# Kernel tuning notes

Measured on AMD Instinct MI355X. Metric: run time of the kernel, lower is better.

The kernel has to match this reference:

```python
import jax, jax.numpy as jnp
import numpy as np

N, E = 100000, 640000
IN, H, C, L = 128, 128, 64, 5
BN_EPS = 1e-5


def setup_inputs() -> dict:
    key = jax.random.key(0)
    ks = jax.random.split(key, 12)
    x = jax.random.normal(ks[0], (N, IN), jnp.float32)
    edge_index = jax.random.randint(ks[1], (2, E), 0, N, dtype=jnp.int64)
    # GCNConv weights: layer0 in->hidden, layers 1..4 hidden->hidden
    W_in = jax.random.normal(ks[2], (IN, H), jnp.float32) / np.sqrt(IN).astype(np.float32)
    b_in = jnp.zeros((H,), jnp.float32)
    Ws = jax.random.normal(ks[3], (L - 1, H, H), jnp.float32) / np.sqrt(H).astype(np.float32)
    bs = jnp.zeros((L - 1, H), jnp.float32)
    # BatchNorm1d (eval mode) params per layer
    gammas = jnp.ones((L, H), jnp.float32)
    betas = jnp.zeros((L, H), jnp.float32)
    run_mean = 0.1 * jax.random.normal(ks[4], (L, H), jnp.float32)
    run_var = jax.random.uniform(ks[5], (L, H), jnp.float32) + 0.5
    # final node-level classifier
    W_out = jax.random.normal(ks[6], (H, C), jnp.float32) / np.sqrt(H).astype(np.float32)
    b_out = jnp.zeros((C,), jnp.float32)
    return {"x": x, "edge_index": edge_index, "W_in": W_in, "b_in": b_in,
            "Ws": Ws, "bs": bs, "gammas": gammas, "betas": betas,
            "run_mean": run_mean, "run_var": run_var, "W_out": W_out, "b_out": b_out}


def reference(x, edge_index, W_in, b_in, Ws, bs, gammas, betas, run_mean, run_var, W_out, b_out):
    src, dst = edge_index[0], edge_index[1]
    n = x.shape[0]
    # GCN symmetric norm with self-loops: deg counts incoming edges + 1
    deg = jax.ops.segment_sum(jnp.ones(src.shape, x.dtype), dst, num_segments=n) + 1.0
    dis = jax.lax.rsqrt(deg)                      # deg^{-1/2}, [N]
    coef = dis[src] * dis[dst]                    # per-edge norm, [E]
    self_coef = (dis * dis)[:, None]              # self-loop norm deg^{-1}, [N,1]

    h = x
    for l in range(L):
        W = W_in if l == 0 else Ws[l - 1]
        b = b_in if l == 0 else bs[l - 1]
        t = h @ W                                 # [N,H]
        agg = jax.ops.segment_sum(t[src] * coef[:, None], dst, num_segments=n)
        agg = agg + t * self_coef + b             # neighbor agg + self loop + bias
        # BatchNorm1d in eval mode (running stats)
        y = (agg - run_mean[l]) * jax.lax.rsqrt(run_var[l] + BN_EPS) * gammas[l] + betas[l]
        h = jax.nn.relu(y)                        # dropout is identity in eval
    return h @ W_out + b_out                      # [N, num_classes]
```

## Files before the change

### kernel.cpp

```cpp
#include <hip/hip_runtime.h>
#include <cstdint>

#define BN_EPS 1e-5f

typedef __bf16 bf16x8 __attribute__((ext_vector_type(8)));
typedef __bf16 bf16x4 __attribute__((ext_vector_type(4)));
typedef __bf16 bf16x2 __attribute__((ext_vector_type(2)));
typedef float f32x4 __attribute__((ext_vector_type(4)));


__global__ __launch_bounds__(256) void k_count(const int* __restrict__ dstv,
                                               int* __restrict__ counts,
                                               int* __restrict__ rank, int E) {
  int e = blockIdx.x * 256 + threadIdx.x;
  if (e < E) rank[e] = atomicAdd(counts + dstv[e], 1);
}

__global__ __launch_bounds__(256) void k_dis(const int* __restrict__ counts,
                                             float* __restrict__ dis, int N) {
  int i = blockIdx.x * 256 + threadIdx.x;
  if (i < N) dis[i] = rsqrtf((float)counts[i] + 1.0f);
}

__global__ __launch_bounds__(256) void k_scan1(const int* __restrict__ counts,
                                               int* __restrict__ rowstart,
                                               int* __restrict__ bsum, int N) {
  __shared__ int wsum[4];
  const int tid = threadIdx.x, lane = tid & 63, wv = tid >> 6;
  const int base = blockIdx.x * 1024 + tid * 4;
  int c[4];
#pragma unroll
  for (int j = 0; j < 4; ++j) {
    int idx = base + j;
    c[j] = (idx < N) ? counts[idx] : 0;
  }
  int s = c[0] + c[1] + c[2] + c[3];
  int x = s;
  for (int d = 1; d < 64; d <<= 1) {
    int y = __shfl_up(x, d);
    if (lane >= d) x += y;
  }
  if (lane == 63) wsum[wv] = x;
  __syncthreads();
  int woff = 0;
  for (int w = 0; w < wv; ++w) woff += wsum[w];
  int r = woff + x - s;
#pragma unroll
  for (int j = 0; j < 4; ++j) {
    int idx = base + j;
    if (idx < N) rowstart[idx] = r;
    r += c[j];
  }
  if (tid == 255) bsum[blockIdx.x] = woff + x;
}

__global__ __launch_bounds__(256) void k_scan2(const int* __restrict__ bsum,
                                               int* __restrict__ boff, int nb) {
  __shared__ int sm[256];
  const int tid = threadIdx.x;
  int v = (tid < nb) ? bsum[tid] : 0;
  sm[tid] = v;
  __syncthreads();
  for (int d = 1; d < 256; d <<= 1) {
    int y = (tid >= d) ? sm[tid - d] : 0;
    __syncthreads();
    sm[tid] += y;
    __syncthreads();
  }
  if (tid < nb) boff[tid] = sm[tid] - v;
}

__global__ __launch_bounds__(256) void k_fix(int* __restrict__ rowstart,
                                             const int* __restrict__ boff, int N) {
  int i = blockIdx.x * 256 + threadIdx.x;
  if (i < N) rowstart[i] += boff[i >> 10];
}

__global__ __launch_bounds__(256) void k_scatter(const int* __restrict__ src,
                                                 const int* __restrict__ dstv,
                                                 const int* __restrict__ rowstart,
                                                 const int* __restrict__ rank,
                                                 int* __restrict__ esrc, int E) {
  int e = blockIdx.x * 256 + threadIdx.x;
  if (e < E) esrc[rowstart[dstv[e]] + rank[e]] = src[e];
}

__global__ __launch_bounds__(256) void k_bnparam(const float* __restrict__ gamma,
                                                 const float* __restrict__ beta,
                                                 const float* __restrict__ mean,
                                                 const float* __restrict__ var,
                                                 float* __restrict__ scale,
                                                 float* __restrict__ shift, int n) {
  int i = blockIdx.x * 256 + threadIdx.x;
  if (i < n) {
    float s = gamma[i] * rsqrtf(var[i] + BN_EPS);
    scale[i] = s;
    shift[i] = beta[i] - mean[i] * s;
  }
}

__global__ __launch_bounds__(64) void k_zrow(__bf16* __restrict__ t, int N) {
  bf16x2 z;
  z[0] = (__bf16)0.f;
  z[1] = (__bf16)0.f;
  *reinterpret_cast<bf16x2*>(t + (size_t)N * 128 + threadIdx.x * 2) = z;
}

__global__ __launch_bounds__(256) void k_wprep(const float* __restrict__ W_in,
                                               const float* __restrict__ Ws,
                                               const float* __restrict__ W_out,
                                               __bf16* __restrict__ wfrag) {
  const int idx = blockIdx.x * 256 + threadIdx.x;
  if (idx >= 11264) return;
  int l, r, CT;
  if (idx < 10240) { l = idx >> 11; r = idx & 2047; CT = 8; }
  else             { l = 5; r = idx - 10240; CT = 4; }
  const int lane = r & 63;
  const int rr = r >> 6;
  const int ct = rr % CT;
  const int kc_i = rr / CT;
  const int lr = lane & 15, kg = lane >> 4;
  const int col = ct * 16 + lr;
  const int k0 = kc_i * 32 + kg * 8;
  const float* Wsrc;
  int ncols;
  if (l == 0)      { Wsrc = W_in; ncols = 128; }
  else if (l <= 4) { Wsrc = Ws + (size_t)(l - 1) * 16384; ncols = 128; }
  else             { Wsrc = W_out; ncols = 64; }
  bf16x8 hi, lo;
#pragma unroll
  for (int j = 0; j < 8; ++j) {
    float v = Wsrc[(size_t)(k0 + j) * ncols + col];
    __bf16 h = (__bf16)v;
    hi[j] = h;
    lo[j] = (__bf16)(v - (float)h);
  }
  const size_t lbase = (l < 5) ? (size_t)l * 65536 : (size_t)327680;
  char* outp = (char*)wfrag + lbase;
  *(bf16x8*)(outp + ((size_t)(kc_i * 2 + 0) * CT + ct) * 1024 + lane * 16) = hi;
  *(bf16x8*)(outp + ((size_t)(kc_i * 2 + 1) * CT + ct) * 1024 + lane * 16) = lo;
}

__global__ __launch_bounds__(256, 4) void k_mgemm0(
    const float* __restrict__ in, const __bf16* __restrict__ wfrag,
    const float* __restrict__ dis, __bf16* __restrict__ outh, int N) {
  constexpr int CT = 8;
  __shared__ __align__(16) char Abase[32768];

  const int tid = threadIdx.x;
  const int lane = tid & 63;
  const int wv = tid >> 6;
  const int lr = lane & 15;
  const int kg = lane >> 4;
  const int rowBase = blockIdx.x * 128;

  {
    const int kq = tid & 31;
#pragma unroll
    for (int i = 0; i < 16; ++i) {
      const int row = (tid >> 5) + i * 8;
      const int grow = rowBase + row;
      float4 v = make_float4(0.f, 0.f, 0.f, 0.f);
      if (grow < N) v = *(const float4*)(in + (size_t)grow * 128 + kq * 4);
      bf16x4 h;
      h[0] = (__bf16)v.x; h[1] = (__bf16)v.y; h[2] = (__bf16)v.z; h[3] = (__bf16)v.w;
      int byte = row * 256 + kq * 8;
      byte ^= (row & 7) << 4;
      *(bf16x4*)(Abase + byte) = h;
    }
  }
  __syncthreads();

  f32x4 acc[2][CT] = {};
#pragma unroll
  for (int kc_i = 0; kc_i < 4; ++kc_i) {
    bf16x8 afr[2];
#pragma unroll
    for (int rt = 0; rt < 2; ++rt) {
      const int row = wv * 32 + rt * 16 + lr;
      int byte = row * 256 + kc_i * 64 + kg * 16;
      byte ^= (row & 7) << 4;
      afr[rt] = *(const bf16x8*)(Abase + byte);
    }
    const char* wk = (const char*)wfrag + (size_t)kc_i * (2 * CT * 1024) +
                     (size_t)lane * 16;
#pragma unroll
    for (int ct = 0; ct < CT; ++ct) {
      bf16x8 bhi = *(const bf16x8*)(wk + ct * 1024);
      bf16x8 blo = *(const bf16x8*)(wk + (CT + ct) * 1024);
#pragma unroll
      for (int rt = 0; rt < 2; ++rt) {
        acc[rt][ct] = __builtin_amdgcn_mfma_f32_16x16x32_bf16(afr[rt], bhi,
                                                              acc[rt][ct], 0, 0, 0);
        acc[rt][ct] = __builtin_amdgcn_mfma_f32_16x16x32_bf16(afr[rt], blo,
                                                              acc[rt][ct], 0, 0, 0);
      }
    }
  }

#pragma unroll
  for (int rt = 0; rt < 2; ++rt) {
#pragma unroll
    for (int j = 0; j < 4; ++j) {
      const int row = rowBase + wv * 32 + rt * 16 + kg * 4 + j;
      if (row < N) {
        const float dr = dis[row];
#pragma unroll
        for (int ct = 0; ct < CT; ++ct)
          outh[(size_t)row * 128 + ct * 16 + lr] = (__bf16)(acc[rt][ct][j] * dr);
      }
    }
  }
}

template <int CT, bool FINAL>
__global__ __launch_bounds__(256, 6) void k_layer(
    const __bf16* __restrict__ tin, const __bf16* __restrict__ wfrag,
    const int* __restrict__ rowstart, const int* __restrict__ counts,
    const int* __restrict__ esrc, const float* __restrict__ dis,
    const float* __restrict__ bias, const float* __restrict__ scale,
    const float* __restrict__ shift, const float* __restrict__ out_bias,
    float* __restrict__ outf, __bf16* __restrict__ outh, int N) {
  __shared__ __align__(16) char Abase[16384];

  const int tid = threadIdx.x;
  const int lane = tid & 63;
  const int wv = tid >> 6;
  const int lr = lane & 15;
  const int kg = lane >> 4;
  const int rowBase = blockIdx.x * 64;

  {
    const int nb0 = rowBase + wv * 16;
    int mb = 0, mc = 0, mdbits = 0;
    if (lane < 16) {
      const int nd = nb0 + lane;
      if (nd < N) {
        mb = rowstart[nd];
        mc = counts[nd];
        mdbits = __float_as_int(dis[nd]);
      }
    }
    const int f0 = lane * 2;
    const float bx = bias[f0], by = bias[f0 + 1];
    const float scx = scale[f0], scy = scale[f0 + 1];
    const float shx = shift[f0], shy = shift[f0 + 1];

    int ci = __builtin_amdgcn_readlane(mc, 0);
    int rec = (lane < ci) ? esrc[__builtin_amdgcn_readlane(mb, 0) + lane] : N;

    for (int i = 0; i < 16; ++i) {
      const int node = nb0 + i;
      const float dn = __int_as_float(__builtin_amdgcn_readlane(mdbits, i));
      const int srow = (node < N) ? node : N;
      const bf16x2 sv =
          *reinterpret_cast<const bf16x2*>(tin + (size_t)srow * 128 + f0);
      int rec_n = N, cn = 0;
      if (i < 15) {
        const int bn_ = __builtin_amdgcn_readlane(mb, i + 1);
        cn = __builtin_amdgcn_readlane(mc, i + 1);
        if (lane < cn) rec_n = esrc[bn_ + lane];
      }
      float ax = (float)sv[0];
      float ay = (float)sv[1];
      const int m = ci < 64 ? ci : 64;
      const int rounds = (m + 7) >> 3;
      for (int r = 0; r < rounds; ++r) {
        const int rb = r * 8;
#pragma unroll
        for (int u = 0; u < 8; ++u) {
          const int s = __builtin_amdgcn_readlane(rec, rb + u);
          const bf16x2 v =
              *reinterpret_cast<const bf16x2*>(tin + (size_t)s * 128 + f0);
          ax += (float)v[0];
          ay += (float)v[1];
        }
      }
      if (__builtin_expect(ci > 64, 0)) {
        const int bi = __builtin_amdgcn_readlane(mb, i);
        for (int e = 64; e < ci; ++e) {
          const int s0 = esrc[bi + e];
          const bf16x2 v0 =
              *reinterpret_cast<const bf16x2*>(tin + (size_t)s0 * 128 + f0);
          ax += (float)v0[0];
          ay += (float)v0[1];
        }
      }
      ax = fmaf(ax, dn, bx);
      ay = fmaf(ay, dn, by);
      ax = fmaxf(fmaf(ax, scx, shx), 0.f);
      ay = fmaxf(fmaf(ay, scy, shy), 0.f);
      bf16x2 o;
      o[0] = (__bf16)ax;
      o[1] = (__bf16)ay;
      const int row = wv * 16 + i;
      int byte = row * 256 + lane * 4;
      byte ^= (row & 7) << 4;
      *(bf16x2*)(Abase + byte) = o;
      rec = rec_n;
      ci = cn;
    }
  }
  __threadfence_block();

  f32x4 acc[CT] = {};
#pragma unroll
  for (int kc_i = 0; kc_i < 4; ++kc_i) {
    const int row = wv * 16 + lr;
    int byte = row * 256 + kc_i * 64 + kg * 16;
    byte ^= (row & 7) << 4;
    const bf16x8 afr = *(const bf16x8*)(Abase + byte);
    const char* wk = (const char*)wfrag + (size_t)kc_i * (2 * CT * 1024) +
                     (size_t)lane * 16;
#pragma unroll
    for (int ct = 0; ct < CT; ++ct) {
      bf16x8 bhi = *(const bf16x8*)(wk + ct * 1024);
      bf16x8 blo = *(const bf16x8*)(wk + (CT + ct) * 1024);
      acc[ct] = __builtin_amdgcn_mfma_f32_16x16x32_bf16(afr, bhi, acc[ct], 0, 0, 0);
      acc[ct] = __builtin_amdgcn_mfma_f32_16x16x32_bf16(afr, blo, acc[ct], 0, 0, 0);
    }
  }

  float ob[CT];
  if constexpr (FINAL) {
#pragma unroll
    for (int ct = 0; ct < CT; ++ct) ob[ct] = out_bias[ct * 16 + lr];
  }
#pragma unroll
  for (int j = 0; j < 4; ++j) {
    const int row = rowBase + wv * 16 + kg * 4 + j;
    if (row < N) {
      if constexpr (FINAL) {
#pragma unroll
        for (int ct = 0; ct < CT; ++ct)
          outf[(size_t)row * (CT * 16) + ct * 16 + lr] = acc[ct][j] + ob[ct];
      } else {
        const float dr = dis[row];
#pragma unroll
        for (int ct = 0; ct < CT; ++ct)
          outh[(size_t)row * 128 + ct * 16 + lr] = (__bf16)(acc[ct][j] * dr);
      }
    }
  }
}

extern "C" void kernel_launch(void* const* d_in, const int* in_sizes, int n_in,
                              void* d_out, int out_size, void* d_ws, size_t ws_size,
                              hipStream_t stream) {
  const float* x      = (const float*)d_in[0];
  const int*   ei     = (const int*)d_in[1];
  const float* W_in   = (const float*)d_in[2];
  const float* b_in   = (const float*)d_in[3];
  const float* Ws     = (const float*)d_in[4];
  const float* bs     = (const float*)d_in[5];
  const float* gammas = (const float*)d_in[6];
  const float* betas  = (const float*)d_in[7];
  const float* mean   = (const float*)d_in[8];
  const float* var    = (const float*)d_in[9];
  const float* W_out  = (const float*)d_in[10];
  const float* b_out  = (const float*)d_in[11];
  float* out = (float*)d_out;

  const int N = in_sizes[0] / 128;
  const int E = in_sizes[1] / 2;
  const int* src = ei;
  const int* dst = ei + E;

  char* ws = (char*)d_ws;
  size_t off = 0;
  auto alloc = [&](size_t bytes) {
    void* p = ws + off;
    off = (off + bytes + 255) & ~255ULL;
    return p;
  };
  int*    counts   = (int*)alloc((size_t)N * 4);
  int*    rowstart = (int*)alloc((size_t)N * 4);
  int*    bsum     = (int*)alloc(256 * 4);
  int*    boff     = (int*)alloc(256 * 4);
  float*  dis      = (float*)alloc((size_t)N * 4);
  float*  scale    = (float*)alloc(5 * 128 * 4);
  float*  shift    = (float*)alloc(5 * 128 * 4);
  __bf16* wfrag    = (__bf16*)alloc(360448);
  int*    rank     = (int*)alloc((size_t)E * 4);
  int*    esrc     = (int*)alloc((size_t)E * 4);
  __bf16* tA       = (__bf16*)alloc(((size_t)N + 1) * 128 * 2);
  __bf16* tB       = (__bf16*)alloc(((size_t)N + 1) * 128 * 2);
  (void)ws_size;

  const int nb = (N + 1023) / 1024;

  hipMemsetAsync(counts, 0, (size_t)N * 4, stream);
  k_count<<<(E + 255) / 256, 256, 0, stream>>>(dst, counts, rank, E);
  k_dis<<<(N + 255) / 256, 256, 0, stream>>>(counts, dis, N);
  k_scan1<<<nb, 256, 0, stream>>>(counts, rowstart, bsum, N);
  k_scan2<<<1, 256, 0, stream>>>(bsum, boff, nb);
  k_fix<<<(N + 255) / 256, 256, 0, stream>>>(rowstart, boff, N);
  k_scatter<<<(E + 255) / 256, 256, 0, stream>>>(src, dst, rowstart, rank, esrc, E);
  k_bnparam<<<(5 * 128 + 255) / 256, 256, 0, stream>>>(gammas, betas, mean, var,
                                                       scale, shift, 5 * 128);
  k_wprep<<<44, 256, 0, stream>>>(W_in, Ws, W_out, wfrag);
  k_zrow<<<1, 64, 0, stream>>>(tA, N);
  k_zrow<<<1, 64, 0, stream>>>(tB, N);

  const int gblocks = (N + 127) / 128;
  const int lblocks = (N + 63) / 64;

  k_mgemm0<<<gblocks, 256, 0, stream>>>(x, wfrag, dis, tA, N);

  const float* biases[5] = {b_in, bs, bs + 128, bs + 256, bs + 384};
  __bf16* tin = tA;
  __bf16* tout = tB;
  for (int l = 1; l <= 4; ++l) {
    k_layer<8, false><<<lblocks, 256, 0, stream>>>(
        tin, wfrag + (size_t)l * 32768, rowstart, counts, esrc, dis,
        biases[l - 1], scale + (l - 1) * 128, shift + (l - 1) * 128, nullptr,
        nullptr, tout, N);
    __bf16* tmp = tin;
    tin = tout;
    tout = tmp;
  }
  k_layer<4, true><<<lblocks, 256, 0, stream>>>(
      tin, wfrag + 163840, rowstart, counts, esrc, dis, biases[4],
      scale + 4 * 128, shift + 4 * 128, b_out, out, nullptr, N);
}
```

Before: 293.4 us.

## Merge setup kernels and gather two nodes' neighbors concurrently in layer kernel

Folds degree-normalization into the scan kernel and combines the weight prep, BN parameter, and zero-row kernels into one launch, cutting four kernel launches. In the layer kernel's aggregation, two destination nodes are processed per iteration, with the first eight neighbor rows of each issued up front to raise memory-level parallelism. Nodes with more than eight neighbors fall back to the original round loop. The unrolled gathers add register pressure and may reduce occupancy.

```diff
diff --git a/kernel.cpp b/kernel.cpp
--- a/kernel.cpp
+++ b/kernel.cpp
@@ -16,15 +16,10 @@
   if (e < E) rank[e] = atomicAdd(counts + dstv[e], 1);
 }
 
-__global__ __launch_bounds__(256) void k_dis(const int* __restrict__ counts,
-                                             float* __restrict__ dis, int N) {
-  int i = blockIdx.x * 256 + threadIdx.x;
-  if (i < N) dis[i] = rsqrtf((float)counts[i] + 1.0f);
-}
-
 __global__ __launch_bounds__(256) void k_scan1(const int* __restrict__ counts,
                                                int* __restrict__ rowstart,
-                                               int* __restrict__ bsum, int N) {
+                                               int* __restrict__ bsum,
+                                               float* __restrict__ dis, int N) {
   __shared__ int wsum[4];
   const int tid = threadIdx.x, lane = tid & 63, wv = tid >> 6;
   const int base = blockIdx.x * 1024 + tid * 4;
@@ -33,6 +28,7 @@
   for (int j = 0; j < 4; ++j) {
     int idx = base + j;
     c[j] = (idx < N) ? counts[idx] : 0;
+    if (idx < N) dis[idx] = rsqrtf((float)c[j] + 1.0f);
   }
   int s = c[0] + c[1] + c[2] + c[3];
   int x = s;
@@ -85,60 +81,56 @@
   if (e < E) esrc[rowstart[dstv[e]] + rank[e]] = src[e];
 }
 
-__global__ __launch_bounds__(256) void k_bnparam(const float* __restrict__ gamma,
-                                                 const float* __restrict__ beta,
-                                                 const float* __restrict__ mean,
-                                                 const float* __restrict__ var,
-                                                 float* __restrict__ scale,
-                                                 float* __restrict__ shift, int n) {
-  int i = blockIdx.x * 256 + threadIdx.x;
-  if (i < n) {
-    float s = gamma[i] * rsqrtf(var[i] + BN_EPS);
+__global__ __launch_bounds__(256) void k_prep(
+    const float* __restrict__ W_in, const float* __restrict__ Ws,
+    const float* __restrict__ W_out, __bf16* __restrict__ wfrag,
+    const float* __restrict__ gamma, const float* __restrict__ beta,
+    const float* __restrict__ mean, const float* __restrict__ var,
+    float* __restrict__ scale, float* __restrict__ shift,
+    __bf16* __restrict__ tA, __bf16* __restrict__ tB, int N) {
+  const int idx = blockIdx.x * 256 + threadIdx.x;
+  if (idx < 11264) {
+    int l, r, CT;
+    if (idx < 10240) { l = idx >> 11; r = idx & 2047; CT = 8; }
+    else             { l = 5; r = idx - 10240; CT = 4; }
+    const int lane = r & 63;
+    const int rr = r >> 6;
+    const int ct = rr % CT;
+    const int kc_i = rr / CT;
+    const int lr = lane & 15, kg = lane >> 4;
+    const int col = ct * 16 + lr;
+    const int k0 = kc_i * 32 + kg * 8;
+    const float* Wsrc;
+    int ncols;
+    if (l == 0)      { Wsrc = W_in; ncols = 128; }
+    else if (l <= 4) { Wsrc = Ws + (size_t)(l - 1) * 16384; ncols = 128; }
+    else             { Wsrc = W_out; ncols = 64; }
+    bf16x8 hi, lo;
+#pragma unroll
+    for (int j = 0; j < 8; ++j) {
+      float v = Wsrc[(size_t)(k0 + j) * ncols + col];
+      __bf16 h = (__bf16)v;
+      hi[j] = h;
+      lo[j] = (__bf16)(v - (float)h);
+    }
+    const size_t lbase = (l < 5) ? (size_t)l * 65536 : (size_t)327680;
+    char* outp = (char*)wfrag + lbase;
+    *(bf16x8*)(outp + ((size_t)(kc_i * 2 + 0) * CT + ct) * 1024 + lane * 16) = hi;
+    *(bf16x8*)(outp + ((size_t)(kc_i * 2 + 1) * CT + ct) * 1024 + lane * 16) = lo;
+  } else if (idx < 11904) {
+    const int i = idx - 11264;
+    const float s = gamma[i] * rsqrtf(var[i] + BN_EPS);
     scale[i] = s;
     shift[i] = beta[i] - mean[i] * s;
-  }
-}
-
-__global__ __launch_bounds__(64) void k_zrow(__bf16* __restrict__ t, int N) {
-  bf16x2 z;
-  z[0] = (__bf16)0.f;
-  z[1] = (__bf16)0.f;
-  *reinterpret_cast<bf16x2*>(t + (size_t)N * 128 + threadIdx.x * 2) = z;
-}
-
-__global__ __launch_bounds__(256) void k_wprep(const float* __restrict__ W_in,
-                                               const float* __restrict__ Ws,
-                                               const float* __restrict__ W_out,
-                                               __bf16* __restrict__ wfrag) {
-  const int idx = blockIdx.x * 256 + threadIdx.x;
-  if (idx >= 11264) return;
-  int l, r, CT;
-  if (idx < 10240) { l = idx >> 11; r = idx & 2047; CT = 8; }
-  else             { l = 5; r = idx - 10240; CT = 4; }
-  const int lane = r & 63;
-  const int rr = r >> 6;
-  const int ct = rr % CT;
-  const int kc_i = rr / CT;
-  const int lr = lane & 15, kg = lane >> 4;
-  const int col = ct * 16 + lr;
-  const int k0 = kc_i * 32 + kg * 8;
-  const float* Wsrc;
-  int ncols;
-  if (l == 0)      { Wsrc = W_in; ncols = 128; }
-  else if (l <= 4) { Wsrc = Ws + (size_t)(l - 1) * 16384; ncols = 128; }
-  else             { Wsrc = W_out; ncols = 64; }
-  bf16x8 hi, lo;
-#pragma unroll
-  for (int j = 0; j < 8; ++j) {
-    float v = Wsrc[(size_t)(k0 + j) * ncols + col];
-    __bf16 h = (__bf16)v;
-    hi[j] = h;
-    lo[j] = (__bf16)(v - (float)h);
-  }
-  const size_t lbase = (l < 5) ? (size_t)l * 65536 : (size_t)327680;
-  char* outp = (char*)wfrag + lbase;
-  *(bf16x8*)(outp + ((size_t)(kc_i * 2 + 0) * CT + ct) * 1024 + lane * 16) = hi;
-  *(bf16x8*)(outp + ((size_t)(kc_i * 2 + 1) * CT + ct) * 1024 + lane * 16) = lo;
+  } else if (idx < 11968) {
+    const int lane = idx - 11904;
+    bf16x2 z; z[0] = (__bf16)0.f; z[1] = (__bf16)0.f;
+    *reinterpret_cast<bf16x2*>(tA + (size_t)N * 128 + lane * 2) = z;
+  } else if (idx < 12032) {
+    const int lane = idx - 11968;
+    bf16x2 z; z[0] = (__bf16)0.f; z[1] = (__bf16)0.f;
+    *reinterpret_cast<bf16x2*>(tB + (size_t)N * 128 + lane * 2) = z;
+  }
 }
 
 __global__ __launch_bounds__(256, 4) void k_mgemm0(
@@ -246,59 +238,127 @@
     const float scx = scale[f0], scy = scale[f0 + 1];
     const float shx = shift[f0], shy = shift[f0 + 1];
 
-    int ci = __builtin_amdgcn_readlane(mc, 0);
-    int rec = (lane < ci) ? esrc[__builtin_amdgcn_readlane(mb, 0) + lane] : N;
-
-    for (int i = 0; i < 16; ++i) {
-      const int node = nb0 + i;
-      const float dn = __int_as_float(__builtin_amdgcn_readlane(mdbits, i));
-      const int srow = (node < N) ? node : N;
-      const bf16x2 sv =
-          *reinterpret_cast<const bf16x2*>(tin + (size_t)srow * 128 + f0);
-      int rec_n = N, cn = 0;
-      if (i < 15) {
-        const int bn_ = __builtin_amdgcn_readlane(mb, i + 1);
-        cn = __builtin_amdgcn_readlane(mc, i + 1);
-        if (lane < cn) rec_n = esrc[bn_ + lane];
-      }
-      float ax = (float)sv[0];
-      float ay = (float)sv[1];
-      const int m = ci < 64 ? ci : 64;
-      const int rounds = (m + 7) >> 3;
-      for (int r = 0; r < rounds; ++r) {
-        const int rb = r * 8;
-#pragma unroll
-        for (int u = 0; u < 8; ++u) {
-          const int s = __builtin_amdgcn_readlane(rec, rb + u);
-          const bf16x2 v =
-              *reinterpret_cast<const bf16x2*>(tin + (size_t)s * 128 + f0);
-          ax += (float)v[0];
-          ay += (float)v[1];
+    int c0 = __builtin_amdgcn_readlane(mc, 0);
+    int c1 = __builtin_amdgcn_readlane(mc, 1);
+    int rec0 = (lane < c0) ? esrc[__builtin_amdgcn_readlane(mb, 0) + lane] : N;
+    int rec1 = (lane < c1) ? esrc[__builtin_amdgcn_readlane(mb, 1) + lane] : N;
+
+    for (int i = 0; i < 16; i += 2) {
+      const int node0 = nb0 + i, node1 = nb0 + i + 1;
+      const int sr0 = (node0 < N) ? node0 : N;
+      const int sr1 = (node1 < N) ? node1 : N;
+      const bf16x2 sv0 = *(const bf16x2*)(tin + (size_t)sr0 * 128 + f0);
+      const bf16x2 sv1 = *(const bf16x2*)(tin + (size_t)sr1 * 128 + f0);
+
+      bf16x2 g0[8], g1[8];
+#pragma unroll
+      for (int u = 0; u < 8; ++u) {
+        const int s = __builtin_amdgcn_readlane(rec0, u);
+        g0[u] = *(const bf16x2*)(tin + (size_t)s * 128 + f0);
+      }
+#pragma unroll
+      for (int u = 0; u < 8; ++u) {
+        const int s = __builtin_amdgcn_readlane(rec1, u);
+        g1[u] = *(const bf16x2*)(tin + (size_t)s * 128 + f0);
+      }
+
+      int recn0 = N, recn1 = N, cn0 = 0, cn1 = 0;
+      if (i < 14) {
+        cn0 = __builtin_amdgcn_readlane(mc, i + 2);
+        cn1 = __builtin_amdgcn_readlane(mc, i + 3);
+        const int bn0 = __builtin_amdgcn_readlane(mb, i + 2);
+        const int bn1 = __builtin_amdgcn_readlane(mb, i + 3);
+        if (lane < cn0) recn0 = esrc[bn0 + lane];
+        if (lane < cn1) recn1 = esrc[bn1 + lane];
+      }
+
+      float ax = (float)sv0[0], ay = (float)sv0[1];
+#pragma unroll
+      for (int u = 0; u < 8; ++u) {
+        ax += (float)g0[u][0];
+        ay += (float)g0[u][1];
+      }
+      if (__builtin_expect(c0 > 8, 0)) {
+        const int m = c0 < 64 ? c0 : 64;
+        for (int rb = 8; rb < m; rb += 8) {
+#pragma unroll
+          for (int u = 0; u < 8; ++u) {
+            const int s = __builtin_amdgcn_readlane(rec0, rb + u);
+            const bf16x2 v = *(const bf16x2*)(tin + (size_t)s * 128 + f0);
+            ax += (float)v[0];
+            ay += (float)v[1];
+          }
         }
-      }
-      if (__builtin_expect(ci > 64, 0)) {
-        const int bi = __builtin_amdgcn_readlane(mb, i);
-        for (int e = 64; e < ci; ++e) {
-          const int s0 = esrc[bi + e];
-          const bf16x2 v0 =
-              *reinterpret_cast<const bf16x2*>(tin + (size_t)s0 * 128 + f0);
-          ax += (float)v0[0];
-          ay += (float)v0[1];
+        if (c0 > 64) {
+          const int bi = __builtin_amdgcn_readlane(mb, i);
+          for (int e = 64; e < c0; ++e) {
+            const int s0 = esrc[bi + e];
+            const bf16x2 v0 = *(const bf16x2*)(tin + (size_t)s0 * 128 + f0);
+            ax += (float)v0[0];
+            ay += (float)v0[1];
+          }
         }
       }
-      ax = fmaf(ax, dn, bx);
-      ay = fmaf(ay, dn, by);
-      ax = fmaxf(fmaf(ax, scx, shx), 0.f);
-      ay = fmaxf(fmaf(ay, scy, shy), 0.f);
-      bf16x2 o;
-      o[0] = (__bf16)ax;
-      o[1] = (__bf16)ay;
-      const int row = wv * 16 + i;
-      int byte = row * 256 + lane * 4;
-      byte ^= (row & 7) << 4;
-      *(bf16x2*)(Abase + byte) = o;
-      rec = rec_n;
-      ci = cn;
+      {
+        const float dn = __int_as_float(__builtin_amdgcn_readlane(mdbits, i));
+        float tx = fmaf(ax, dn, bx), ty = fmaf(ay, dn, by);
+        tx = fmaxf(fmaf(tx, scx, shx), 0.f);
+        ty = fmaxf(fmaf(ty, scy, shy), 0.f);
+        bf16x2 o;
+        o[0] = (__bf16)tx;
+        o[1] = (__bf16)ty;
+        const int row = wv * 16 + i;
+        int byte = row * 256 + lane * 4;
+        byte ^= (row & 7) << 4;
+        *(bf16x2*)(Abase + byte) = o;
+      }
+
+      ax = (float)sv1[0];
+      ay = (float)sv1[1];
+#pragma unroll
+      for (int u = 0; u < 8; ++u) {
+        ax += (float)g1[u][0];
+        ay += (float)g1[u][1];
+      }
+      if (__builtin_expect(c1 > 8, 0)) {
+        const int m = c1 < 64 ? c1 : 64;
+        for (int rb = 8; rb < m; rb += 8) {
+#pragma unroll
+          for (int u = 0; u < 8; ++u) {
+            const int s = __builtin_amdgcn_readlane(rec1, rb + u);
+            const bf16x2 v = *(const bf16x2*)(tin + (size_t)s * 128 + f0);
+            ax += (float)v[0];
+            ay += (float)v[1];
+          }
+        }
+        if (c1 > 64) {
+          const int bi = __builtin_amdgcn_readlane(mb, i + 1);
+          for (int e = 64; e < c1; ++e) {
+            const int s0 = esrc[bi + e];
+            const bf16x2 v0 = *(const bf16x2*)(tin + (size_t)s0 * 128 + f0);
+            ax += (float)v0[0];
+            ay += (float)v0[1];
+          }
+        }
+      }
+      {
+        const float dn = __int_as_float(__builtin_amdgcn_readlane(mdbits, i + 1));
+        float tx = fmaf(ax, dn, bx), ty = fmaf(ay, dn, by);
+        tx = fmaxf(fmaf(tx, scx, shx), 0.f);
+        ty = fmaxf(fmaf(ty, scy, shy), 0.f);
+        bf16x2 o;
+        o[0] = (__bf16)tx;
+        o[1] = (__bf16)ty;
+        const int row = wv * 16 + i + 1;
+        int byte = row * 256 + lane * 4;
+        byte ^= (row & 7) << 4;
+        *(bf16x2*)(Abase + byte) = o;
+      }
+
+      rec0 = recn0;
+      rec1 = recn1;
+      c0 = cn0;
+      c1 = cn1;
     }
   }
   __threadfence_block();
@@ -391,16 +451,12 @@
 
   hipMemsetAsync(counts, 0, (size_t)N * 4, stream);
   k_count<<<(E + 255) / 256, 256, 0, stream>>>(dst, counts, rank, E);
-  k_dis<<<(N + 255) / 256, 256, 0, stream>>>(counts, dis, N);
-  k_scan1<<<nb, 256, 0, stream>>>(counts, rowstart, bsum, N);
+  k_scan1<<<nb, 256, 0, stream>>>(counts, rowstart, bsum, dis, N);
   k_scan2<<<1, 256, 0, stream>>>(bsum, boff, nb);
   k_fix<<<(N + 255) / 256, 256, 0, stream>>>(rowstart, boff, N);
   k_scatter<<<(E + 255) / 256, 256, 0, stream>>>(src, dst, rowstart, rank, esrc, E);
-  k_bnparam<<<(5 * 128 + 255) / 256, 256, 0, stream>>>(gammas, betas, mean, var,
-                                                       scale, shift, 5 * 128);
-  k_wprep<<<44, 256, 0, stream>>>(W_in, Ws, W_out, wfrag);
-  k_zrow<<<1, 64, 0, stream>>>(tA, N);
-  k_zrow<<<1, 64, 0, stream>>>(tB, N);
+  k_prep<<<47, 256, 0, stream>>>(W_in, Ws, W_out, wfrag, gammas, betas, mean, var,
+                                 scale, shift, tA, tB, N);
 
   const int gblocks = (N + 127) / 128;
   const int lblocks = (N + 63) / 64;
```

New measurement: 285.5 us. 2.7% less time.
